# Optimization experiments

Hardware: AMD Instinct MI355X
Metric: run time of the kernel (lower is better)

The kernel has to match this reference:

```python
import jax, jax.numpy as jnp
import numpy as np

IN_FEATURES = 8192
OUT_FEATURES = 8192
BATCH_TOKENS = 64
QMAX = 255  # uint8-style storage range


def setup_inputs() -> dict:
    key = jax.random.key(0)
    k_x, k_w, k_s, k_z, k_b = jax.random.split(key, 5)
    x = jax.random.normal(k_x, (BATCH_TOKENS, IN_FEATURES), dtype=jnp.float32)
    # quantized weight stored as integer codes in [0, 255], per-output-channel qparams
    qweight = jax.random.randint(k_w, (OUT_FEATURES, IN_FEATURES), 0, QMAX + 1, dtype=jnp.int32)
    scales = jax.random.uniform(k_s, (OUT_FEATURES,), dtype=jnp.float32, minval=0.001, maxval=0.02)
    zero_points = jax.random.randint(k_z, (OUT_FEATURES,), 100, 156, dtype=jnp.int32)
    bias = jax.random.normal(k_b, (OUT_FEATURES,), dtype=jnp.float32)
    return {"x": x, "qweight": qweight, "scales": scales, "zero_points": zero_points, "bias": bias}


def reference(x, qweight, scales, zero_points, bias):
    # Dequantize per-output-channel affine quantized weight: W = (q - zp) * scale
    # qweight: [out, in], scales/zero_points: [out]
    w = (qweight.astype(jnp.float32) - zero_points.astype(jnp.float32)[:, None]) * scales[:, None]
    # y = x @ W^T + b : [tokens, out]
    return jnp.einsum('ti,oi->to', x, w) + bias
```

## Files before the change

kernel.cpp:

```cpp
#include <hip/hip_runtime.h>
#include <hip/hip_fp16.h>

#define T_DIM 64
#define K_DIM 8192
#define N_DIM 8192
#define KSPLIT 16
#define KC (K_DIM / KSPLIT)
#define BN 128

typedef __fp16 half8_t __attribute__((ext_vector_type(8)));
typedef __fp16 half4_t __attribute__((ext_vector_type(4)));
typedef __fp16 half2_t __attribute__((ext_vector_type(2)));
typedef float  f32x4   __attribute__((ext_vector_type(4)));
typedef int    i32x4   __attribute__((ext_vector_type(4)));

__global__ __launch_bounds__(256) void prep_kernel(const float* __restrict__ x,
                                                   __fp16* __restrict__ xh,
                                                   float* __restrict__ rowsum) {
    const int t = blockIdx.x;
    const float* xr = x + (size_t)t * K_DIM;
    __fp16* xhr = xh + (size_t)t * K_DIM;
    float s = 0.0f;
    for (int k = threadIdx.x * 4; k < K_DIM; k += 256 * 4) {
        f32x4 v = *(const f32x4*)(xr + k);
        half4_t h;
        h[0] = (__fp16)v[0]; h[1] = (__fp16)v[1];
        h[2] = (__fp16)v[2]; h[3] = (__fp16)v[3];
        *(half4_t*)(xhr + k) = h;
        s += (float)h[0] + (float)h[1] + (float)h[2] + (float)h[3];
    }
    #pragma unroll
    for (int off = 32; off > 0; off >>= 1) s += __shfl_down(s, off, 64);
    __shared__ float red[4];
    const int lane = threadIdx.x & 63;
    const int w = threadIdx.x >> 6;
    if (lane == 0) red[w] = s;
    __syncthreads();
    if (threadIdx.x == 0) rowsum[t] = red[0] + red[1] + red[2] + red[3];
}

__global__ __launch_bounds__(256, 4) void woq_gemm_kernel(
        const int* __restrict__ qw, const __fp16* __restrict__ xh,
        const float* __restrict__ rowsum, const float* __restrict__ scales,
        const int* __restrict__ zps, const float* __restrict__ bias,
        float* __restrict__ out) {
    const int bx = blockIdx.x;
    const int bz = blockIdx.y;
    const int tid = threadIdx.x;
    const int wid = __builtin_amdgcn_readfirstlane(tid >> 6);
    const int lane = tid & 63;
    const int r = lane & 15;
    const int g = lane >> 4;

    const int n_wave = bx * BN + wid * 32;
    const int k0 = bz * KC;

    const __fp16* aptr = xh + (size_t)r * K_DIM + k0 + g * 8;
    const int* bptr = qw + (size_t)(n_wave + r) * K_DIM + k0 + g * 8;

    f32x4 acc[4][2] = {};

    #pragma unroll 2
    for (int kk = 0; kk < KC; kk += 32) {
        half8_t af[4];
        #pragma unroll
        for (int m = 0; m < 4; ++m)
            af[m] = *(const half8_t*)(aptr + (size_t)m * 16 * K_DIM + kk);

        half8_t bf[2];
        #pragma unroll
        for (int n = 0; n < 2; ++n) {
            const int* bp = bptr + (size_t)n * 16 * K_DIM + kk;
            i32x4 q0 = *(const i32x4*)bp;
            i32x4 q1 = *(const i32x4*)(bp + 4);
            union { half8_t h8; half2_t h2[4]; } u;
            u.h2[0] = __builtin_amdgcn_cvt_pkrtz((float)q0[0], (float)q0[1]);
            u.h2[1] = __builtin_amdgcn_cvt_pkrtz((float)q0[2], (float)q0[3]);
            u.h2[2] = __builtin_amdgcn_cvt_pkrtz((float)q1[0], (float)q1[1]);
            u.h2[3] = __builtin_amdgcn_cvt_pkrtz((float)q1[2], (float)q1[3]);
            bf[n] = u.h8;
        }

        #pragma unroll
        for (int m = 0; m < 4; ++m)
            #pragma unroll
            for (int n = 0; n < 2; ++n)
                acc[m][n] = __builtin_amdgcn_mfma_f32_16x16x32_f16(af[m], bf[n], acc[m][n], 0, 0, 0);
    }

    #pragma unroll
    for (int n = 0; n < 2; ++n) {
        const int c = n_wave + n * 16 + r;
        const float sc = scales[c];
        const float szp = sc * (float)zps[c];
        const float bv = bias[c];
        #pragma unroll
        for (int m = 0; m < 4; ++m) {
            #pragma unroll
            for (int j = 0; j < 4; ++j) {
                const int t = m * 16 + g * 4 + j;
                float val = sc * acc[m][n][j];
                if (bz == 0) val += bv - szp * rowsum[t];
                atomicAdd(&out[(size_t)t * N_DIM + c], val);
            }
        }
    }
}

extern "C" void kernel_launch(void* const* d_in, const int* in_sizes, int n_in,
                              void* d_out, int out_size, void* d_ws, size_t ws_size,
                              hipStream_t stream) {
    const float* x      = (const float*)d_in[0];
    const int*   qw     = (const int*)d_in[1];
    const float* scales = (const float*)d_in[2];
    const int*   zps    = (const int*)d_in[3];
    const float* bias   = (const float*)d_in[4];
    float* out = (float*)d_out;

    __fp16* xh  = (__fp16*)d_ws;
    float* rowsum = (float*)((char*)d_ws + (size_t)T_DIM * K_DIM * sizeof(__fp16));

    (void)hipMemsetAsync(d_out, 0, (size_t)out_size * sizeof(float), stream);
    prep_kernel<<<T_DIM, 256, 0, stream>>>(x, xh, rowsum);
    woq_gemm_kernel<<<dim3(N_DIM / BN, KSPLIT), 256, 0, stream>>>(
        qw, xh, rowsum, scales, zps, bias, out);
}
```

Before: 406.2 us.

## Replace split-K atomics with partial buffers and a separate reduce kernel

The GEMM kernel now writes its split-K partial accumulators to a workspace buffer in a lane-contiguous layout instead of issuing atomicAdds to the output. A new reduce kernel sums the 16 partials with vector loads and applies scale, zero-point correction and bias. This also removes the output memset. The prep kernel is spread over 4x more blocks with partial row sums. The cost is an extra 32 MB of partial-buffer writes and reads plus one more kernel launch, in exchange for dropping 8M scattered atomics.

```diff
diff --git a/kernel.cpp b/kernel.cpp
--- a/kernel.cpp
+++ b/kernel.cpp
@@ -7,6 +7,7 @@
 #define KSPLIT 16
 #define KC (K_DIM / KSPLIT)
 #define BN 128
+#define NBX (N_DIM / BN)
 
 typedef __fp16 half8_t __attribute__((ext_vector_type(8)));
 typedef __fp16 half4_t __attribute__((ext_vector_type(4)));
@@ -16,19 +17,24 @@
 
 __global__ __launch_bounds__(256) void prep_kernel(const float* __restrict__ x,
                                                    __fp16* __restrict__ xh,
-                                                   float* __restrict__ rowsum) {
-    const int t = blockIdx.x;
-    const float* xr = x + (size_t)t * K_DIM;
-    __fp16* xhr = xh + (size_t)t * K_DIM;
+                                                   float* __restrict__ rowsum_part) {
+    const int t = blockIdx.x >> 2;
+    const int q = blockIdx.x & 3;
+    const int kbase = q * (K_DIM / 4) + threadIdx.x * 8;
+    const float* xr = x + (size_t)t * K_DIM + kbase;
+    __fp16* xhr = xh + (size_t)t * K_DIM + kbase;
+
+    f32x4 v0 = *(const f32x4*)xr;
+    f32x4 v1 = *(const f32x4*)(xr + 4);
+    half8_t h;
+    h[0] = (__fp16)v0[0]; h[1] = (__fp16)v0[1]; h[2] = (__fp16)v0[2]; h[3] = (__fp16)v0[3];
+    h[4] = (__fp16)v1[0]; h[5] = (__fp16)v1[1]; h[6] = (__fp16)v1[2]; h[7] = (__fp16)v1[3];
+    *(half8_t*)xhr = h;
+
     float s = 0.0f;
-    for (int k = threadIdx.x * 4; k < K_DIM; k += 256 * 4) {
-        f32x4 v = *(const f32x4*)(xr + k);
-        half4_t h;
-        h[0] = (__fp16)v[0]; h[1] = (__fp16)v[1];
-        h[2] = (__fp16)v[2]; h[3] = (__fp16)v[3];
-        *(half4_t*)(xhr + k) = h;
-        s += (float)h[0] + (float)h[1] + (float)h[2] + (float)h[3];
-    }
+    #pragma unroll
+    for (int i = 0; i < 8; ++i) s += (float)h[i];
+
     #pragma unroll
     for (int off = 32; off > 0; off >>= 1) s += __shfl_down(s, off, 64);
     __shared__ float red[4];
@@ -36,14 +42,12 @@
     const int w = threadIdx.x >> 6;
     if (lane == 0) red[w] = s;
     __syncthreads();
-    if (threadIdx.x == 0) rowsum[t] = red[0] + red[1] + red[2] + red[3];
+    if (threadIdx.x == 0) rowsum_part[t * 4 + q] = red[0] + red[1] + red[2] + red[3];
 }
 
 __global__ __launch_bounds__(256, 4) void woq_gemm_kernel(
         const int* __restrict__ qw, const __fp16* __restrict__ xh,
-        const float* __restrict__ rowsum, const float* __restrict__ scales,
-        const int* __restrict__ zps, const float* __restrict__ bias,
-        float* __restrict__ out) {
+        float* __restrict__ part) {
     const int bx = blockIdx.x;
     const int bz = blockIdx.y;
     const int tid = threadIdx.x;
@@ -88,23 +92,49 @@
                 acc[m][n] = __builtin_amdgcn_mfma_f32_16x16x32_f16(af[m], bf[n], acc[m][n], 0, 0, 0);
     }
 
+    float* pp = part + (((size_t)bz * NBX + bx) * 4 + wid) * 2048 + g * 16 + r;
     #pragma unroll
-    for (int n = 0; n < 2; ++n) {
-        const int c = n_wave + n * 16 + r;
-        const float sc = scales[c];
-        const float szp = sc * (float)zps[c];
-        const float bv = bias[c];
+    for (int n = 0; n < 2; ++n)
         #pragma unroll
-        for (int m = 0; m < 4; ++m) {
+        for (int m = 0; m < 4; ++m)
             #pragma unroll
-            for (int j = 0; j < 4; ++j) {
-                const int t = m * 16 + g * 4 + j;
-                float val = sc * acc[m][n][j];
-                if (bz == 0) val += bv - szp * rowsum[t];
-                atomicAdd(&out[(size_t)t * N_DIM + c], val);
-            }
-        }
-    }
+            for (int j = 0; j < 4; ++j)
+                pp[((n * 4 + m) * 4 + j) * 64] = acc[m][n][j];
+}
+
+__global__ __launch_bounds__(256) void reduce_kernel(
+        const float* __restrict__ part, const float* __restrict__ rowsum_part,
+        const float* __restrict__ scales, const int* __restrict__ zps,
+        const float* __restrict__ bias, float* __restrict__ out) {
+    const int idx = blockIdx.x * 256 + threadIdx.x;
+    const int e = idx * 4;
+    const int t = e >> 13;
+    const int c = e & (N_DIM - 1);
+    const int bx = c >> 7;
+    const int wid = (c >> 5) & 3;
+    const int n = (c >> 4) & 1;
+    const int r0 = c & 15;
+    const int m = t >> 4;
+    const int g = (t >> 2) & 3;
+    const int j = t & 3;
+
+    const size_t off = ((size_t)bx * 4 + wid) * 2048 + ((n * 4 + m) * 4 + j) * 64 + g * 16 + r0;
+    f32x4 s = {0.f, 0.f, 0.f, 0.f};
+    #pragma unroll
+    for (int bz = 0; bz < KSPLIT; ++bz)
+        s += *(const f32x4*)(part + (size_t)bz * (NBX * 4 * 2048) + off);
+
+    const float rs = rowsum_part[t * 4 + 0] + rowsum_part[t * 4 + 1] +
+                     rowsum_part[t * 4 + 2] + rowsum_part[t * 4 + 3];
+
+    f32x4 sc = *(const f32x4*)(scales + c);
+    i32x4 zp = *(const i32x4*)(zps + c);
+    f32x4 bv = *(const f32x4*)(bias + c);
+    f32x4 y;
+    #pragma unroll
+    for (int i = 0; i < 4; ++i)
+        y[i] = sc[i] * (s[i] - (float)zp[i] * rs) + bv[i];
+    *(f32x4*)(out + e) = y;
 }
 
 extern "C" void kernel_launch(void* const* d_in, const int* in_sizes, int n_in,
@@ -117,11 +147,12 @@
     const float* bias   = (const float*)d_in[4];
     float* out = (float*)d_out;
 
-    __fp16* xh  = (__fp16*)d_ws;
-    float* rowsum = (float*)((char*)d_ws + (size_t)T_DIM * K_DIM * sizeof(__fp16));
+    __fp16* xh          = (__fp16*)d_ws;
+    float*  rowsum_part = (float*)((char*)d_ws + (size_t)T_DIM * K_DIM * sizeof(__fp16));
+    float*  part        = (float*)((char*)d_ws + (2u << 20));
 
-    (void)hipMemsetAsync(d_out, 0, (size_t)out_size * sizeof(float), stream);
-    prep_kernel<<<T_DIM, 256, 0, stream>>>(x, xh, rowsum);
-    woq_gemm_kernel<<<dim3(N_DIM / BN, KSPLIT), 256, 0, stream>>>(
-        qw, xh, rowsum, scales, zps, bias, out);
+    prep_kernel<<<256, 256, 0, stream>>>(x, xh, rowsum_part);
+    woq_gemm_kernel<<<dim3(NBX, KSPLIT), 256, 0, stream>>>(qw, xh, part);
+    reduce_kernel<<<(T_DIM * N_DIM / 4) / 256, 256, 0, stream>>>(
+        part, rowsum_part, scales, zps, bias, out);
 }
```

Measured after the change: 389.4 us. 1.04x faster.
